# Kernel tuning notes

Hardware: AMD Instinct MI355X
Metric: run time of the kernel (lower is better)

The kernel has to match this reference:

```python
import jax, jax.numpy as jnp
import numpy as np

GAMMA = 0.1   # gl.gamma
BIG = 1e10    # stand-in for +inf in the DP border (keeps grads NaN-free)


def _softdtw(D, gamma=GAMMA):
    """Soft-DTW value for a batch of cost matrices D: [B, T, T] -> [B].
    R[i,j] = D[i,j] + softmin_gamma(R[i-1,j-1], R[i-1,j], R[i,j-1]).
    Vectorized over the batch; sequential DP over rows (outer scan) and
    columns (inner scan), matching the reference recurrence exactly.
    """
    B, T, _ = D.shape
    dt = D.dtype
    # R[0, :] = [0, inf, inf, ...]  (length T+1, padded border)
    prev = jnp.concatenate([jnp.zeros((B, 1), dt), jnp.full((B, T), BIG, dt)], axis=1)

    def col_step(r_left, xs):
        d, r_diag, r_up = xs  # each [B]
        stacked = jnp.stack([r_diag, r_up, r_left])  # [3, B]
        r = d - gamma * jax.nn.logsumexp(-stacked / gamma, axis=0)
        return r, r

    def row_step(prev_row, d_row):  # prev_row [B, T+1], d_row [B, T]
        xs = (d_row.T, prev_row[:, :-1].T, prev_row[:, 1:].T)  # each [T, B]
        _, rows = jax.lax.scan(col_step, jnp.full((B,), BIG, dt), xs)  # [T, B]
        new_row = jnp.concatenate([jnp.full((B, 1), BIG, dt), rows.T], axis=1)
        return new_row, None

    final_row, _ = jax.lax.scan(row_step, prev, jnp.swapaxes(D, 0, 1))
    return final_row[:, -1]  # R[T, T]


def setup_inputs() -> dict:
    key = jax.random.key(0)
    n_class, n_support, n_query, t, c = 20, 5, 25, 32, 2048
    n = n_class * (n_support + n_query)
    inp = jax.random.normal(key, (n, t, c), jnp.float32)
    # episode labels, grouped per class (as produced by an episodic sampler)
    target = jnp.repeat(jnp.arange(n_class, dtype=jnp.int32), n_support + n_query)
    return {"inp": inp, "target": target, "n_support": n_support, "n_class": n_class}


def reference(inp, target, n_support, n_class):
    n, t, c = inp.shape
    per_class = n // n_class
    n_query = per_class - n_support

    # group samples by class (stable sort == torch.nonzero(target.eq(c)) ordering)
    order = jnp.argsort(target, stable=True)
    grouped = inp[order].reshape(n_class, per_class, t, c)
    z_proto = grouped[:, :n_support].mean(axis=1)                 # [m, t, c]
    zq = grouped[:, n_support:].reshape(n_class * n_query, t, c)  # [nq, t, c]

    # pairwise squared-Euclidean frame costs (no [nq*m, t, c] expansion)
    x2 = jnp.sum(zq * zq, axis=-1)          # [nq, t]
    y2 = jnp.sum(z_proto * z_proto, axis=-1)  # [m, t]
    xy = jnp.einsum('nic,mjc->nmij', zq, z_proto)  # [nq, m, t, t]
    cost_xy = x2[:, None, :, None] + y2[None, :, None, :] - 2.0 * xy
    nq, m = cost_xy.shape[:2]
    d_xy = _softdtw(cost_xy.reshape(nq * m, t, t)).reshape(nq, m)

    # normalization terms: D(x,x), D(y,y)
    cxx = x2[:, :, None] + x2[:, None, :] - 2.0 * jnp.einsum('nic,njc->nij', zq, zq)
    cyy = y2[:, :, None] + y2[:, None, :] - 2.0 * jnp.einsum('mic,mjc->mij', z_proto, z_proto)
    d_xx = _softdtw(cxx)  # [nq]
    d_yy = _softdtw(cyy)  # [m]
    dist = d_xy - 0.5 * (d_xx[:, None] + d_yy[None, :])  # [nq, m]

    log_p_y = jax.nn.log_softmax(-dist, axis=1).reshape(n_class, n_query, n_class)
    tgt = jnp.broadcast_to(jnp.arange(n_class)[:, None, None], (n_class, n_query, 1))
    batch_loss = -jnp.take_along_axis(log_p_y, tgt, axis=2).reshape(-1)
    loss_val = batch_loss.mean()
    y_hat = jnp.argmax(log_p_y, axis=2)
    acc_val = (y_hat == tgt[..., 0]).astype(jnp.float32).mean()
    return loss_val, acc_val, batch_loss
```

## Files before the change

kernel.cpp:

```cpp
#include <hip/hip_runtime.h>

#define T 32
#define C 2048
#define NTOT 600
#define NCLASS 20
#define NSUP 5
#define PER 30
#define NQPC 25
#define NQ 500
#define NQROWS (NQ * T)
#define NPROWS (NCLASS * T)
#define GAMMA 0.1f
#define INVG 10.0f
#define BIG 1e10f
#define NMM (NQ * NCLASS + NQ + NCLASS)
#define GEMM_BLKS 625
#define SYRK_BLKS_PAD 136
#define STAGE_BLKS_A 2000
#define STAGE_BLKS_B 80

typedef __fp16 half8 __attribute__((ext_vector_type(8)));
typedef float f32x4 __attribute__((ext_vector_type(4)));

__global__ __launch_bounds__(640) void sort_kernel(const int* __restrict__ target,
                                                   int* __restrict__ order,
                                                   int* __restrict__ qsrc) {
    __shared__ int tgt[NTOT];
    __shared__ int offs[NCLASS];
    __shared__ int ordl[NTOT];
    int tid = threadIdx.x;
    if (tid < NTOT) tgt[tid] = target[tid];
    __syncthreads();
    if (tid < NCLASS) {
        int o = 0;
        for (int i = 0; i < NTOT; i++) o += (tgt[i] < tid) ? 1 : 0;
        offs[tid] = o;
    }
    __syncthreads();
    if (tid < NTOT) {
        int c = tgt[tid];
        int rank = 0;
        for (int k = 0; k < NTOT; k++) rank += (k < tid && tgt[k] == c) ? 1 : 0;
        ordl[offs[c] + rank] = tid;
    }
    __syncthreads();
    if (tid < NTOT) order[tid] = ordl[tid];
    if (tid < NQ) qsrc[tid] = ordl[(tid / NQPC) * PER + NSUP + (tid % NQPC)];
}

__global__ __launch_bounds__(512) void stage_kernel(const float* __restrict__ inp,
                                                    const int* __restrict__ qsrc,
                                                    const int* __restrict__ order,
                                                    half8* __restrict__ Ah,
                                                    half8* __restrict__ Bh) {
    int bid = blockIdx.x;
    int tid = threadIdx.x;
    int row = tid & 15, seg = tid >> 4;
    bool isA = bid < STAGE_BLKS_A;
    int b = isA ? bid : bid - STAGE_BLKS_A;
    int rowblk = b >> 1, half = b & 1;
    int rowg = rowblk * 16 + row;
    int col0 = half * 1024 + seg * 32;
    int chunk0 = half * 128 + seg * 4;
    float vals[32];
    if (isA) {
        const float* src = inp + (size_t)qsrc[rowg >> 5] * (T * C) + (size_t)(rowg & 31) * C + col0;
#pragma unroll
        for (int i = 0; i < 8; i++) {
            float4 v = *(const float4*)(src + i * 4);
            vals[i * 4 + 0] = v.x; vals[i * 4 + 1] = v.y;
            vals[i * 4 + 2] = v.z; vals[i * 4 + 3] = v.w;
        }
        half8 hv[4];
#pragma unroll
        for (int e = 0; e < 32; e++) hv[e >> 3][e & 7] = (__fp16)vals[e];
#pragma unroll
        for (int c = 0; c < 4; c++) Ah[(size_t)(chunk0 + c) * NQROWS + rowg] = hv[c];
    } else {
        int cls = rowg >> 5, trow = rowg & 31;
        const float* base = inp + (size_t)trow * C + col0;
        const float* s0 = base + (size_t)order[cls * PER + 0] * (T * C);
        const float* s1 = base + (size_t)order[cls * PER + 1] * (T * C);
        const float* s2 = base + (size_t)order[cls * PER + 2] * (T * C);
        const float* s3 = base + (size_t)order[cls * PER + 3] * (T * C);
        const float* s4 = base + (size_t)order[cls * PER + 4] * (T * C);
#pragma unroll
        for (int i = 0; i < 8; i++) {
            float4 a = *(const float4*)(s0 + i * 4);
            float4 b4 = *(const float4*)(s1 + i * 4);
            float4 c = *(const float4*)(s2 + i * 4);
            float4 d = *(const float4*)(s3 + i * 4);
            float4 e = *(const float4*)(s4 + i * 4);
            vals[i * 4 + 0] = (a.x + b4.x + c.x + d.x + e.x) * 0.2f;
            vals[i * 4 + 1] = (a.y + b4.y + c.y + d.y + e.y) * 0.2f;
            vals[i * 4 + 2] = (a.z + b4.z + c.z + d.z + e.z) * 0.2f;
            vals[i * 4 + 3] = (a.w + b4.w + c.w + d.w + e.w) * 0.2f;
        }
        half8 hv[4];
#pragma unroll
        for (int e = 0; e < 32; e++) hv[e >> 3][e & 7] = (__fp16)vals[e];
#pragma unroll
        for (int c = 0; c < 4; c++) Bh[(size_t)(chunk0 + c) * NPROWS + rowg] = hv[c];
    }
}

__global__ __launch_bounds__(256) void gemm_syrk_kernel(const half8* __restrict__ Ah,
                                                        const half8* __restrict__ Bh,
                                                        float* __restrict__ xy,
                                                        float* __restrict__ gxx,
                                                        float* __restrict__ gyy) {
    int tid = threadIdx.x, lane = tid & 63, wid = tid >> 6;
    int o = blockIdx.x;
    int g = lane >> 4, r = lane & 15;
    if (o < SYRK_BLKS_PAD) {
        int ww = o * 4 + wid;
        if (ww >= NQ + NCLASS) return;
        const half8* hi;
        int nrows, row0;
        float* outp;
        if (ww < NQ) {
            hi = Ah; nrows = NQROWS; row0 = ww * 32;
            outp = gxx + (size_t)ww * (T * T);
        } else {
            hi = Bh; nrows = NPROWS; row0 = (ww - NQ) * 32;
            outp = gyy + (size_t)(ww - NQ) * (T * T);
        }
        f32x4 acc[2][2];
        f32x4 zero = {0.f, 0.f, 0.f, 0.f};
        acc[0][0] = zero; acc[0][1] = zero; acc[1][0] = zero; acc[1][1] = zero;
        for (int t = 0; t < C / 32; t++) {
            size_t base = (size_t)(t * 4 + g) * nrows + row0 + r;
            half8 h0 = hi[base], h1 = hi[base + 16];
            acc[0][0] = __builtin_amdgcn_mfma_f32_16x16x32_f16(h0, h0, acc[0][0], 0, 0, 0);
            acc[0][1] = __builtin_amdgcn_mfma_f32_16x16x32_f16(h0, h1, acc[0][1], 0, 0, 0);
            acc[1][0] = __builtin_amdgcn_mfma_f32_16x16x32_f16(h1, h0, acc[1][0], 0, 0, 0);
            acc[1][1] = __builtin_amdgcn_mfma_f32_16x16x32_f16(h1, h1, acc[1][1], 0, 0, 0);
        }
#pragma unroll
        for (int mi = 0; mi < 2; mi++)
#pragma unroll
            for (int ni = 0; ni < 2; ni++)
#pragma unroll
                for (int j = 0; j < 4; j++)
                    outp[(mi * 16 + g * 4 + j) * T + ni * 16 + r] = acc[mi][ni][j];
        return;
    }
    int oo = o - SYRK_BLKS_PAD;
    int xcd = oo & 7, slot = oo >> 3;
    int v = (xcd < 1 ? xcd * 79 : 79 + (xcd - 1) * 78) + slot;
    int bm = v / 5, bn = v % 5;
    int wr = wid >> 1, wc = wid & 1;
    int m0 = bm * 128 + wr * 64, n0 = bn * 128 + wc * 64;
    const half8* pA = Ah + (size_t)g * NQROWS + m0 + r;
    const half8* pB = Bh + (size_t)g * NPROWS + n0 + r;
    f32x4 acc[4][4];
    f32x4 zero = {0.f, 0.f, 0.f, 0.f};
#pragma unroll
    for (int mi = 0; mi < 4; mi++)
#pragma unroll
        for (int ni = 0; ni < 4; ni++) acc[mi][ni] = zero;
#pragma unroll 2
    for (int t = 0; t < C / 32; t++) {
        half8 ah[4], bh[4];
#pragma unroll
        for (int i = 0; i < 4; i++) {
            ah[i] = pA[i * 16];
            bh[i] = pB[i * 16];
        }
        pA += 4 * NQROWS;
        pB += 4 * NPROWS;
#pragma unroll
        for (int mi = 0; mi < 4; mi++)
#pragma unroll
            for (int ni = 0; ni < 4; ni++)
                acc[mi][ni] = __builtin_amdgcn_mfma_f32_16x16x32_f16(ah[mi], bh[ni], acc[mi][ni], 0, 0, 0);
    }
    int orow = m0 + g * 4;
    int ocol = n0 + r;
#pragma unroll
    for (int mi = 0; mi < 4; mi++)
#pragma unroll
        for (int ni = 0; ni < 4; ni++)
#pragma unroll
            for (int j = 0; j < 4; j++)
                xy[(size_t)(orow + mi * 16 + j) * NPROWS + ocol + ni * 16] = acc[mi][ni][j];
}

__global__ void diag_kernel(const float* __restrict__ gxx, const float* __restrict__ gyy,
                            float* __restrict__ x2, float* __restrict__ y2) {
    int i = blockIdx.x * 256 + threadIdx.x;
    if (i < NQROWS) {
        x2[i] = gxx[(size_t)(i >> 5) * (T * T) + (i & 31) * (T + 1)];
    } else if (i < NQROWS + NPROWS) {
        int j = i - NQROWS;
        y2[j] = gyy[(size_t)(j >> 5) * (T * T) + (j & 31) * (T + 1)];
    }
}

__global__ __launch_bounds__(256) void softdtw_wave_kernel(
        const float* __restrict__ xy, const float* __restrict__ gxx,
        const float* __restrict__ gyy, const float* __restrict__ x2,
        const float* __restrict__ y2, float* __restrict__ dxy,
        float* __restrict__ dxx, float* __restrict__ dyy) {
    int tid = threadIdx.x;
    int j = tid & 31;
    int mm = blockIdx.x * 8 + (tid >> 5);
    bool valid = mm < NMM;
    int mmc = valid ? mm : 0;
    const float* rterm;
    const float* cterm;
    const float* cptr;
    int cstride;
    float* outp;
    if (mmc < NQ * NCLASS) {
        int q = mmc / NCLASS, m = mmc % NCLASS;
        rterm = x2 + q * T;
        cterm = y2 + m * T;
        cptr = xy + (size_t)(q * T) * NPROWS + m * T;
        cstride = NPROWS;
        outp = dxy + mmc;
    } else if (mmc < NQ * NCLASS + NQ) {
        int i = mmc - NQ * NCLASS;
        rterm = x2 + i * T;
        cterm = rterm;
        cptr = gxx + (size_t)i * (T * T);
        cstride = T;
        outp = dxx + i;
    } else {
        int i = mmc - NQ * NCLASS - NQ;
        rterm = y2 + i * T;
        cterm = rterm;
        cptr = gyy + (size_t)i * (T * T);
        cstride = T;
        outp = dyy + i;
    }
    float cjv = cterm[j];
    float xreg = rterm[j];
    float my_prev = BIG, my_prev2 = BIG;
    int ip = 0 - j; ip = ip < 0 ? 0 : (ip > 31 ? 31 : ip);
    float nxt_xy = cptr[(size_t)ip * cstride + j];
    for (int k = 0; k < 63; k++) {
        float cur_xy = nxt_xy;
        int in = k + 1 - j; in = in < 0 ? 0 : (in > 31 ? 31 : in);
        nxt_xy = cptr[(size_t)in * cstride + j];
        float lp = __shfl_up(my_prev, 1, 32);
        float dg = __shfl_up(my_prev2, 1, 32);
        if (j == 0) { lp = BIG; dg = (k == 0) ? 0.f : BIG; }
        float up = my_prev;
        int i = k - j;
        float ai = __shfl(xreg, i & 31, 32);
        float d = ai + cjv - 2.0f * cur_xy;
        float mn = fminf(dg, fminf(up, lp));
        float ssum = __expf((mn - dg) * INVG) + __expf((mn - up) * INVG) +
                     __expf((mn - lp) * INVG);
        float r = d + mn - GAMMA * __logf(ssum);
        bool active = (i >= 0) && (i < 32);
        my_prev2 = my_prev;
        my_prev = active ? r : my_prev;
    }
    if (j == 31 && valid) *outp = my_prev;
}

__global__ __launch_bounds__(512) void finalize_kernel(const float* __restrict__ dxy,
                                                       const float* __restrict__ dxx,
                                                       const float* __restrict__ dyy,
                                                       float* __restrict__ out) {
    __shared__ float sl[512];
    __shared__ float sa[512];
    int q = threadIdx.x;
    float bl = 0.f, fl = 0.f;
    if (q < NQ) {
        float dxxq = dxx[q];
        int cq = q / NQPC;
        float dd[NCLASS];
#pragma unroll
        for (int m = 0; m < NCLASS; m++)
            dd[m] = dxy[q * NCLASS + m] - 0.5f * (dxxq + dyy[m]);
        float best = dd[0];
        int bi = 0;
#pragma unroll
        for (int m = 1; m < NCLASS; m++) {
            if (dd[m] < best) { best = dd[m]; bi = m; }
        }
        float s = 0.f;
        float dcq = dd[0];
#pragma unroll
        for (int m = 0; m < NCLASS; m++) {
            s += __expf(best - dd[m]);
            if (m == cq) dcq = dd[m];
        }
        float lse = __logf(s) - best;
        bl = dcq + lse;
        out[2 + q] = bl;
        fl = (bi == cq) ? 1.f : 0.f;
    }
    sl[threadIdx.x] = bl;
    sa[threadIdx.x] = fl;
    __syncthreads();
    for (int off = 256; off; off >>= 1) {
        if (threadIdx.x < off) {
            sl[threadIdx.x] += sl[threadIdx.x + off];
            sa[threadIdx.x] += sa[threadIdx.x + off];
        }
        __syncthreads();
    }
    if (threadIdx.x == 0) {
        out[0] = sl[0] / (float)NQ;
        out[1] = sa[0] / (float)NQ;
    }
}

extern "C" void kernel_launch(void* const* d_in, const int* in_sizes, int n_in,
                              void* d_out, int out_size, void* d_ws, size_t ws_size,
                              hipStream_t stream) {
    const float* inp = (const float*)d_in[0];
    const int* target = (const int*)d_in[1];
    float* out = (float*)d_out;
    char* ws = (char*)d_ws;

    size_t off = 0;
    auto carve = [&](size_t bytes) {
        void* p = ws + off;
        off = (off + bytes + 255) & ~(size_t)255;
        return p;
    };
    int* order = (int*)carve(NTOT * sizeof(int));
    int* qsrc = (int*)carve(NQ * sizeof(int));
    float* x2 = (float*)carve((size_t)NQROWS * sizeof(float));
    float* y2 = (float*)carve((size_t)NPROWS * sizeof(float));
    float* xy = (float*)carve((size_t)NQROWS * NPROWS * sizeof(float));
    float* gxx = (float*)carve((size_t)NQ * T * T * sizeof(float));
    float* gyy = (float*)carve((size_t)NCLASS * T * T * sizeof(float));
    float* dxy = (float*)carve((size_t)NQ * NCLASS * sizeof(float));
    float* dxx = (float*)carve((size_t)NQ * sizeof(float));
    float* dyy = (float*)carve((size_t)NCLASS * sizeof(float));
    half8* Ah = (half8*)carve((size_t)(C / 8) * NQROWS * 16);
    half8* Bh = (half8*)carve((size_t)(C / 8) * NPROWS * 16);
    (void)ws_size;

    sort_kernel<<<1, 640, 0, stream>>>(target, order, qsrc);
    stage_kernel<<<STAGE_BLKS_A + STAGE_BLKS_B, 512, 0, stream>>>(inp, qsrc, order, Ah, Bh);
    gemm_syrk_kernel<<<SYRK_BLKS_PAD + GEMM_BLKS, 256, 0, stream>>>(Ah, Bh, xy, gxx, gyy);
    diag_kernel<<<(NQROWS + NPROWS + 255) / 256, 256, 0, stream>>>(gxx, gyy, x2, y2);
    softdtw_wave_kernel<<<(NMM + 7) / 8, 256, 0, stream>>>(xy, gxx, gyy, x2, y2, dxy, dxx, dyy);
    finalize_kernel<<<1, 512, 0, stream>>>(dxy, dxx, dyy, out);
}
```

Measured before the change: 194.4 us.

## Tile fp16 staging buffers into 16-row blocks contiguous along the K dimension

Measured after the change: 209.4 us. +7.7%, slower.

```diff
diff --git a/kernel.cpp b/kernel.cpp
--- a/kernel.cpp
+++ b/kernel.cpp
@@ -18,6 +18,7 @@
 #define SYRK_BLKS_PAD 136
 #define STAGE_BLKS_A 2000
 #define STAGE_BLKS_B 80
+#define TILE_STRIDE 4096
 
 typedef __fp16 half8 __attribute__((ext_vector_type(8)));
 typedef float f32x4 __attribute__((ext_vector_type(4)));
@@ -75,7 +76,8 @@
 #pragma unroll
         for (int e = 0; e < 32; e++) hv[e >> 3][e & 7] = (__fp16)vals[e];
 #pragma unroll
-        for (int c = 0; c < 4; c++) Ah[(size_t)(chunk0 + c) * NQROWS + rowg] = hv[c];
+        for (int c = 0; c < 4; c++)
+            Ah[(size_t)rowblk * TILE_STRIDE + (size_t)(chunk0 + c) * 16 + row] = hv[c];
     } else {
         int cls = rowg >> 5, trow = rowg & 31;
         const float* base = inp + (size_t)trow * C + col0;
@@ -100,7 +102,8 @@
 #pragma unroll
         for (int e = 0; e < 32; e++) hv[e >> 3][e & 7] = (__fp16)vals[e];
 #pragma unroll
-        for (int c = 0; c < 4; c++) Bh[(size_t)(chunk0 + c) * NPROWS + rowg] = hv[c];
+        for (int c = 0; c < 4; c++)
+            Bh[(size_t)rowblk * TILE_STRIDE + (size_t)(chunk0 + c) * 16 + row] = hv[c];
     }
 }
 
@@ -116,21 +119,22 @@
         int ww = o * 4 + wid;
         if (ww >= NQ + NCLASS) return;
         const half8* hi;
-        int nrows, row0;
+        int row0;
         float* outp;
         if (ww < NQ) {
-            hi = Ah; nrows = NQROWS; row0 = ww * 32;
+            hi = Ah; row0 = ww * 32;
             outp = gxx + (size_t)ww * (T * T);
         } else {
-            hi = Bh; nrows = NPROWS; row0 = (ww - NQ) * 32;
+            hi = Bh; row0 = (ww - NQ) * 32;
             outp = gyy + (size_t)(ww - NQ) * (T * T);
         }
+        const half8* p = hi + (size_t)(row0 >> 4) * TILE_STRIDE + g * 16 + r;
         f32x4 acc[2][2];
         f32x4 zero = {0.f, 0.f, 0.f, 0.f};
         acc[0][0] = zero; acc[0][1] = zero; acc[1][0] = zero; acc[1][1] = zero;
         for (int t = 0; t < C / 32; t++) {
-            size_t base = (size_t)(t * 4 + g) * nrows + row0 + r;
-            half8 h0 = hi[base], h1 = hi[base + 16];
+            half8 h0 = p[0], h1 = p[TILE_STRIDE];
+            p += 64;
             acc[0][0] = __builtin_amdgcn_mfma_f32_16x16x32_f16(h0, h0, acc[0][0], 0, 0, 0);
             acc[0][1] = __builtin_amdgcn_mfma_f32_16x16x32_f16(h0, h1, acc[0][1], 0, 0, 0);
             acc[1][0] = __builtin_amdgcn_mfma_f32_16x16x32_f16(h1, h0, acc[1][0], 0, 0, 0);
@@ -151,8 +155,8 @@
     int bm = v / 5, bn = v % 5;
     int wr = wid >> 1, wc = wid & 1;
     int m0 = bm * 128 + wr * 64, n0 = bn * 128 + wc * 64;
-    const half8* pA = Ah + (size_t)g * NQROWS + m0 + r;
-    const half8* pB = Bh + (size_t)g * NPROWS + n0 + r;
+    const half8* pA = Ah + (size_t)(m0 >> 4) * TILE_STRIDE + g * 16 + r;
+    const half8* pB = Bh + (size_t)(n0 >> 4) * TILE_STRIDE + g * 16 + r;
     f32x4 acc[4][4];
     f32x4 zero = {0.f, 0.f, 0.f, 0.f};
 #pragma unroll
@@ -164,11 +168,11 @@
         half8 ah[4], bh[4];
 #pragma unroll
         for (int i = 0; i < 4; i++) {
-            ah[i] = pA[i * 16];
-            bh[i] = pB[i * 16];
-        }
-        pA += 4 * NQROWS;
-        pB += 4 * NPROWS;
+            ah[i] = pA[(size_t)i * TILE_STRIDE];
+            bh[i] = pB[(size_t)i * TILE_STRIDE];
+        }
+        pA += 64;
+        pB += 64;
 #pragma unroll
         for (int mi = 0; mi < 4; mi++)
 #pragma unroll
```
